# Performance work log

Hardware: AMD Instinct MI355X
Metric: run time of the kernel (lower is better)

The kernel has to match this reference:

```python
import jax, jax.numpy as jnp
import numpy as np

B, T, FDIM, H = 8, 2048, 512, 8
DK = FDIM // H
INF_VAL = 10000.0


def setup_inputs() -> dict:
    key = jax.random.key(0)
    ks = jax.random.split(key, 12)
    s = 1.0 / np.sqrt(FDIM)
    return {
        "query": jax.random.normal(ks[0], (B, T, FDIM), jnp.float32),
        "key": jax.random.normal(ks[1], (B, T, FDIM), jnp.float32),
        "value": jax.random.normal(ks[2], (B, T, FDIM), jnp.float32),
        "mask": jax.random.bernoulli(ks[3], 0.1, (B, T, T)),
        "Wq": jax.random.normal(ks[4], (FDIM, FDIM), jnp.float32) * s,
        "bq": jnp.zeros((FDIM,), jnp.float32),
        "Wk": jax.random.normal(ks[5], (FDIM, FDIM), jnp.float32) * s,
        "bk": jnp.zeros((FDIM,), jnp.float32),
        "Wv": jax.random.normal(ks[6], (FDIM, FDIM), jnp.float32) * s,
        "bv": jnp.zeros((FDIM,), jnp.float32),
        "Wo": jax.random.normal(ks[7], (FDIM, FDIM), jnp.float32) * s,
        "bo": jnp.zeros((FDIM,), jnp.float32),
    }


def reference(query, key, value, mask, Wq, bq, Wk, bk, Wv, bv, Wo, bo):
    # Linear projections (torch Linear: y = x W^T + b) then split heads.
    q = (query @ Wq.T + bq).reshape(B, T, H, DK).transpose(0, 2, 1, 3)  # (B,H,T1,DK)
    k = (key @ Wk.T + bk).reshape(B, T, H, DK).transpose(0, 2, 1, 3)    # (B,H,T2,DK)
    v = (value @ Wv.T + bv).reshape(B, T, H, DK).transpose(0, 2, 1, 3)  # (B,H,T2,DK)
    scores = jnp.einsum("bhqd,bhkd->bhqk", q, k) / jnp.sqrt(jnp.float32(DK))
    m = mask[:, None, :, :]  # (B,1,T1,T2)
    scores = jnp.where(m, -INF_VAL, scores)
    attn = jax.nn.softmax(scores, axis=-1)
    attn = jnp.where(m, 0.0, attn)
    # dropout_rate = 0.0 -> identity
    x = jnp.einsum("bhqk,bhkd->bhqd", attn, v)  # (B,H,T1,DK)
    x = x.transpose(0, 2, 1, 3).reshape(B, T, H * DK)
    return x @ Wo.T + bo
```

## Files before the change

kernel.cpp:

```cpp
#include <hip/hip_runtime.h>
#include <hip/hip_bf16.h>
#include <stdint.h>

#define B_N 8
#define T_N 2048
#define FDIM_N 512
#define H_N 8
#define DK_N 64

typedef float f32x4 __attribute__((ext_vector_type(4)));
typedef float float4v __attribute__((ext_vector_type(4)));
typedef __bf16 bf16x8 __attribute__((ext_vector_type(8)));
typedef unsigned short ushort8v __attribute__((ext_vector_type(8)));
typedef unsigned int uint2v __attribute__((ext_vector_type(2)));
typedef unsigned int uint4v __attribute__((ext_vector_type(4)));

#if __has_builtin(__builtin_amdgcn_exp2f)
#define EXP2F(x) __builtin_amdgcn_exp2f(x)
#else
#define EXP2F(x) exp2f(x)
#endif

static __device__ __forceinline__ unsigned short f2bf(float f) {
  unsigned int u = __builtin_bit_cast(unsigned int, f);
  u += 0x7fffu + ((u >> 16) & 1u);
  return (unsigned short)(u >> 16);
}

static __device__ __forceinline__ unsigned cvtpk(float lo, float hi) {
  unsigned r;
  asm("v_cvt_pk_bf16_f32 %0, %1, %2" : "=v"(r) : "v"(lo), "v"(hi));
  return r;
}

static __device__ __forceinline__ void gld_lds16(const void* g, void* l) {
  __builtin_amdgcn_global_load_lds(
      (const __attribute__((address_space(1))) unsigned int*)g,
      (__attribute__((address_space(3))) unsigned int*)l, 16, 0, 0);
}

static __device__ __forceinline__ bf16x8 ld_bf8(const unsigned short* p) {
  return *reinterpret_cast<const bf16x8*>(p);
}

#define SWZ8(row, colE) ((colE) ^ (((row) & 7) << 3))

#define QSCALE 0.1803368801111244f

__global__ __launch_bounds__(256) void prep_k(const int* __restrict__ m,
                                              const float* __restrict__ w0,
                                              const float* __restrict__ w1,
                                              const float* __restrict__ w2,
                                              const float* __restrict__ w3,
                                              unsigned short* __restrict__ wb,
                                              unsigned long long* __restrict__ mbits) {
  const int bid = blockIdx.x;
  if (bid < 2048) {
    const size_t n = (size_t)B_N * T_N * T_N;
    const size_t stride = (size_t)2048 * 256;
    for (size_t i = (size_t)bid * 256 + threadIdx.x; i < n; i += stride) {
      unsigned long long bl = __ballot(m[i] != 0);
      if ((threadIdx.x & 63) == 0) mbits[i >> 6] = bl;
    }
  } else {
    const int i = (bid - 2048) * 256 + threadIdx.x;
    const int ws = i >> 15, o = i & 32767;
    const float* w = (ws == 0) ? w0 : (ws == 1) ? w1 : (ws == 2) ? w2 : w3;
    const float4v a = *reinterpret_cast<const float4v*>(w + (size_t)o * 8);
    const float4v b = *reinterpret_cast<const float4v*>(w + (size_t)o * 8 + 4);
    const ushort8v out = {f2bf(a.x), f2bf(a.y), f2bf(a.z), f2bf(a.w),
                          f2bf(b.x), f2bf(b.y), f2bf(b.z), f2bf(b.w)};
    *reinterpret_cast<ushort8v*>(wb + (size_t)i * 8) = out;
  }
}

__global__ __launch_bounds__(256, 2) void proj_k(
    const float* __restrict__ qin, const float* __restrict__ kin, const float* __restrict__ vin,
    const unsigned short* __restrict__ wb, const float* __restrict__ bq,
    const float* __restrict__ bk, const float* __restrict__ bv,
    unsigned short* __restrict__ q_scr, unsigned short* __restrict__ k_scr,
    unsigned short* __restrict__ vT_scr) {
  __shared__ unsigned short As[128 * 64];
  __shared__ unsigned short Bs[128 * 64];
  const int tid = threadIdx.x;
  const int lane = tid & 63, w = tid >> 6;
  const int lr = lane & 15, lg = lane >> 4;
  const int swz_rd = (lr & 7) << 3;
  const int id = blockIdx.x;
  const int work = (id & 7) * 192 + (id >> 3);
  const int gb = work / 512;
  const int wk = work - gb * 512;
  const int m0 = (wk >> 2) * 128, n0 = (wk & 3) * 128;
  const int wm = (w & 1) * 64, wn = (w >> 1) * 64;

  const float* Ap = (gb == 0) ? qin : (gb == 1) ? kin : vin;
  const unsigned short* Wp = wb + (size_t)gb * 262144;
  const float* biasp = (gb == 0) ? bq : (gb == 1) ? bk : bv;

  f32x4 acc[4][4];
  const f32x4 z4 = {0.f, 0.f, 0.f, 0.f};
#pragma unroll
  for (int i = 0; i < 4; ++i)
#pragma unroll
    for (int j = 0; j < 4; ++j) acc[i][j] = z4;

  float4v areg[8];
#pragma unroll
  for (int j = 0; j < 8; ++j) {
    const int c = j * 256 + tid;
    areg[j] = *reinterpret_cast<const float4v*>(Ap + (size_t)(m0 + (c >> 4)) * 512 + (c & 15) * 4);
  }

  for (int k0 = 0; k0 < 512; k0 += 64) {
    __syncthreads();
#pragma unroll
    for (int j = 0; j < 8; ++j) {
      const int c = j * 256 + tid;
      const int row = c >> 4, g4 = c & 15;
      const uint2v pk = {cvtpk(areg[j].x, areg[j].y), cvtpk(areg[j].z, areg[j].w)};
      const int eo = row * 64 + (((g4 >> 1) * 8) ^ ((row & 7) << 3)) + (g4 & 1) * 4;
      *reinterpret_cast<uint2v*>(&As[eo]) = pk;
    }
#pragma unroll
    for (int i = 0; i < 4; ++i) {
      const int c = i * 256 + tid;
      const int row = c >> 3, ch = c & 7;
      gld_lds16(Wp + (size_t)(n0 + row) * 512 + k0 + SWZ8(row, ch * 8), &Bs[c * 8]);
    }
    if (k0 < 448) {
#pragma unroll
      for (int j = 0; j < 8; ++j) {
        const int c = j * 256 + tid;
        areg[j] = *reinterpret_cast<const float4v*>(Ap + (size_t)(m0 + (c >> 4)) * 512 + k0 + 64 +
                                                    (c & 15) * 4);
      }
    }
    __syncthreads();
    bf16x8 af[4][2], bw[4][2];
#pragma unroll
    for (int mt = 0; mt < 4; ++mt)
#pragma unroll
      for (int kk = 0; kk < 2; ++kk)
        af[mt][kk] = ld_bf8(&As[(wm + mt * 16 + lr) * 64 + ((kk * 32 + lg * 8) ^ swz_rd)]);
#pragma unroll
    for (int nt = 0; nt < 4; ++nt)
#pragma unroll
      for (int kk = 0; kk < 2; ++kk)
        bw[nt][kk] = ld_bf8(&Bs[(wn + nt * 16 + lr) * 64 + ((kk * 32 + lg * 8) ^ swz_rd)]);
#pragma unroll
    for (int kk = 0; kk < 2; ++kk)
#pragma unroll
      for (int mt = 0; mt < 4; ++mt)
#pragma unroll
        for (int nt = 0; nt < 4; ++nt)
          acc[mt][nt] =
              __builtin_amdgcn_mfma_f32_16x16x32_bf16(af[mt][kk], bw[nt][kk], acc[mt][nt], 0, 0, 0);
  }

#pragma unroll
  for (int nt = 0; nt < 4; ++nt) {
    const int n = n0 + wn + nt * 16 + lr;
    const float bias = biasp[n];
#pragma unroll
    for (int mt = 0; mt < 4; ++mt) {
#pragma unroll
      for (int j = 0; j < 4; ++j) {
        const int m = m0 + wm + mt * 16 + lg * 4 + j;
        float v = acc[mt][nt][j] + bias;
        const int bb = m >> 11, t = m & 2047;
        const int hh = n >> 6, d = n & 63;
        if (gb == 0) {
          v *= QSCALE;
          q_scr[(((size_t)(bb * 8 + hh) * 2048 + t) << 6) + d] = f2bf(v);
        } else if (gb == 1) {
          k_scr[(((size_t)(bb * 8 + hh) * 2048 + t) << 6) + d] = f2bf(v);
        } else {
          const int tp = (t & ~31) | (((t >> 2) & 3) << 3) | (((t >> 4) & 1) << 2) | (t & 3);
          vT_scr[(((size_t)(bb * 8 + hh) * 64 + d) << 11) + tp] = f2bf(v);
        }
      }
    }
  }
}

__global__ __launch_bounds__(256, 2) void attn_k(
    const unsigned short* __restrict__ qg, const unsigned short* __restrict__ kg,
    const unsigned short* __restrict__ vtg, const unsigned long long* __restrict__ mb,
    unsigned short* __restrict__ xg) {
  __shared__ unsigned short Ks[2][64 * 64];
  __shared__ unsigned short Vts[2][64 * 64];

  const int tid = threadIdx.x;
  const int lane = tid & 63, w = tid >> 6;
  const int lr = lane & 15, lg = lane >> 4;
  const int swz_rd = (lr & 7) << 3;
  const int id = blockIdx.x;
  const int work = (id & 7) * 128 + (id >> 3);
  const int bh = work >> 4, qt0 = work & 15;
  const int b = bh >> 3, h = bh & 7;
  const int q0 = qt0 * 128;

  bf16x8 aq[2][2];
#pragma unroll
  for (int qt = 0; qt < 2; ++qt)
#pragma unroll
    for (int kk = 0; kk < 2; ++kk)
      aq[qt][kk] =
          ld_bf8(qg + ((size_t)bh * T_N + q0 + w * 32 + qt * 16 + lr) * DK_N + kk * 32 + lg * 8);

  const int c0 = tid, c1 = 256 + tid;
  const int r0 = c0 >> 3, sw0 = SWZ8(r0, (c0 & 7) * 8);
  const int r1 = c1 >> 3, sw1 = SWZ8(r1, (c1 & 7) * 8);
  const unsigned short* kp0 = kg + (size_t)bh * (T_N * DK_N) + r0 * 64 + sw0;
  const unsigned short* kp1 = kg + (size_t)bh * (T_N * DK_N) + r1 * 64 + sw1;
  const unsigned short* vp0 = vtg + ((size_t)bh * DK_N + r0) * T_N + sw0;
  const unsigned short* vp1 = vtg + ((size_t)bh * DK_N + r1) * T_N + sw1;
  const unsigned long long* mp0 = mb + ((size_t)b * T_N + q0 + w * 32 + lr) * (T_N / 64);
  const unsigned long long* mp1 = mp0 + 16 * (T_N / 64);

  f32x4 OT[2][4];
  float l_run[2] = {0.f, 0.f};
  const f32x4 z4 = {0.f, 0.f, 0.f, 0.f};
#pragma unroll
  for (int qt = 0; qt < 2; ++qt)
#pragma unroll
    for (int dt = 0; dt < 4; ++dt) OT[qt][dt] = z4;

#define STAGE(PB)                       \
  {                                     \
    gld_lds16(kp0, &Ks[PB][c0 * 8]);    \
    gld_lds16(kp1, &Ks[PB][c1 * 8]);    \
    gld_lds16(vp0, &Vts[PB][c0 * 8]);   \
    gld_lds16(vp1, &Vts[PB][c1 * 8]);   \
    kp0 += 4096; kp1 += 4096; vp0 += 64; vp1 += 64; \
  }

  f32x4 ST[2][4];
  bf16x8 pfrag[2][2];
  unsigned long long mc0, mc1, mn0 = 0, mn1 = 0;

#define QKT_BLOCK(CUR)                                                                      \
  {                                                                                         \
    __builtin_amdgcn_s_setprio(1);                                                          \
    _Pragma("unroll") for (int st = 0; st < 4; ++st) {                                      \
      const bf16x8 kb0 = ld_bf8(&Ks[CUR][(st * 16 + lr) * 64 + ((lg * 8) ^ swz_rd)]);       \
      const bf16x8 kb1 = ld_bf8(&Ks[CUR][(st * 16 + lr) * 64 + ((32 + lg * 8) ^ swz_rd)]);  \
      _Pragma("unroll") for (int qt = 0; qt < 2; ++qt) {                                    \
        f32x4 a_ = __builtin_amdgcn_mfma_f32_16x16x32_bf16(kb0, aq[qt][0], z4, 0, 0, 0);    \
        ST[qt][st] = __builtin_amdgcn_mfma_f32_16x16x32_bf16(kb1, aq[qt][1], a_, 0, 0, 0);  \
      }                                                                                     \
    }                                                                                       \
    __builtin_amdgcn_s_setprio(0);                                                          \
  }

#define SOFTMAX_BLOCK()                                                                     \
  {                                                                                         \
    _Pragma("unroll") for (int qt = 0; qt < 2; ++qt) {                                      \
      const unsigned long long mrow = qt ? mc1 : mc0;                                       \
      float sv[4][4], rs4[4];                                                               \
      _Pragma("unroll") for (int st = 0; st < 4; ++st) {                                    \
        const unsigned nib = (unsigned)(mrow >> (st * 16 + lg * 4)) & 0xFu;                 \
        _Pragma("unroll") for (int j = 0; j < 4; ++j) {                                     \
          float e = EXP2F(ST[qt][st][j]);                                                   \
          e = ((nib >> j) & 1u) ? 0.f : e;                                                  \
          sv[st][j] = e;                                                                    \
        }                                                                                   \
        rs4[st] = (sv[st][0] + sv[st][1]) + (sv[st][2] + sv[st][3]);                        \
      }                                                                                     \
      float rs = (rs4[0] + rs4[1]) + (rs4[2] + rs4[3]);                                     \
      rs += __shfl_xor(rs, 16);                                                             \
      rs += __shfl_xor(rs, 32);                                                             \
      l_run[qt] += rs;                                                                      \
      uint4v pk0_, pk1_;                                                                    \
      pk0_.x = cvtpk(sv[0][0], sv[0][1]); pk0_.y = cvtpk(sv[0][2], sv[0][3]);               \
      pk0_.z = cvtpk(sv[1][0], sv[1][1]); pk0_.w = cvtpk(sv[1][2], sv[1][3]);               \
      pk1_.x = cvtpk(sv[2][0], sv[2][1]); pk1_.y = cvtpk(sv[2][2], sv[2][3]);               \
      pk1_.z = cvtpk(sv[3][0], sv[3][1]); pk1_.w = cvtpk(sv[3][2], sv[3][3]);               \
      pfrag[qt][0] = __builtin_bit_cast(bf16x8, pk0_);                                      \
      pfrag[qt][1] = __builtin_bit_cast(bf16x8, pk1_);                                      \
    }                                                                                       \
  }

#define PV_BLOCK(PRV)                                                                       \
  {                                                                                         \
    __builtin_amdgcn_s_setprio(1);                                                          \
    _Pragma("unroll") for (int dt = 0; dt < 4; ++dt) {                                      \
      const bf16x8 v0 = ld_bf8(&Vts[PRV][(dt * 16 + lr) * 64 + ((lg * 8) ^ swz_rd)]);       \
      const bf16x8 v1 = ld_bf8(&Vts[PRV][(dt * 16 + lr) * 64 + ((32 + lg * 8) ^ swz_rd)]);  \
      _Pragma("unroll") for (int qt = 0; qt < 2; ++qt) {                                    \
        f32x4 o_ = __builtin_amdgcn_mfma_f32_16x16x32_bf16(v0, pfrag[qt][0], OT[qt][dt], 0, 0, 0); \
        OT[qt][dt] = __builtin_amdgcn_mfma_f32_16x16x32_bf16(v1, pfrag[qt][1], o_, 0, 0, 0); \
      }                                                                                     \
    }                                                                                       \
    __builtin_amdgcn_s_setprio(0);                                                          \
  }

  STAGE(0);
  mc0 = mp0[0]; mc1 = mp1[0];
  __syncthreads();
  QKT_BLOCK(0);
  STAGE(1);
  mn0 = mp0[1]; mn1 = mp1[1];
  SOFTMAX_BLOCK();
  mc0 = mn0; mc1 = mn1;

#define ITER(KT, CUR, LAST)                     \
  {                                             \
    PV_BLOCK(CUR ^ 1);           \
    __syncthreads();                            \
    QKT_BLOCK(CUR);                \
    if (!(LAST)) {                              \
      STAGE(CUR ^ 1);            \
      mn0 = mp0[(KT) + 1]; mn1 = mp1[(KT) + 1]; \
    }                                           \
    SOFTMAX_BLOCK();             \
    mc0 = mn0; mc1 = mn1;                       \
  }

  ITER(1, 1, 0)
  for (int kt0 = 2; kt0 < 30; kt0 += 2) {
    ITER(kt0, 0, 0)
    ITER(kt0 + 1, 1, 0)
  }
  ITER(30, 0, 0)
  ITER(31, 1, 1)
  PV_BLOCK(1);
#undef ITER
#undef STAGE
#undef QKT_BLOCK
#undef SOFTMAX_BLOCK
#undef PV_BLOCK

#pragma unroll
  for (int qt = 0; qt < 2; ++qt) {
    const float l = l_run[qt];
    const float inv = (l > 0.f) ? 1.f / l : 0.f;
    const int q = q0 + w * 32 + qt * 16 + lr;
#pragma unroll
    for (int dt = 0; dt < 4; ++dt) {
      uint2v o;
      o.x = cvtpk(OT[qt][dt][0] * inv, OT[qt][dt][1] * inv);
      o.y = cvtpk(OT[qt][dt][2] * inv, OT[qt][dt][3] * inv);
      *reinterpret_cast<uint2v*>(xg + ((size_t)(b * T_N + q)) * FDIM_N + h * 64 + dt * 16 +
                                 lg * 4) = o;
    }
  }
}

__global__ __launch_bounds__(256, 3) void gemm_out_k(const unsigned short* __restrict__ Ap,
                                                     const unsigned short* __restrict__ Wp,
                                                     const float* __restrict__ biasp,
                                                     float* __restrict__ Cp) {
  __shared__ unsigned short As[128 * 64];
  __shared__ unsigned short Bs[128 * 64];
  const int tid = threadIdx.x;
  const int lane = tid & 63, w = tid >> 6;
  const int lr = lane & 15, lg = lane >> 4;
  const int id = blockIdx.x;
  const int work = (id & 7) * 64 + (id >> 3);
  const int m0 = (work >> 2) * 128, n0 = (work & 3) * 128;
  const int wm = (w & 1) * 64, wn = (w >> 1) * 64;
  const int swz_rd = (lr & 7) << 3;

  f32x4 acc[4][4];
  const f32x4 z4 = {0.f, 0.f, 0.f, 0.f};
#pragma unroll
  for (int i = 0; i < 4; ++i)
#pragma unroll
    for (int j = 0; j < 4; ++j) acc[i][j] = z4;

  for (int k0 = 0; k0 < 512; k0 += 64) {
    __syncthreads();
#pragma unroll
    for (int i = 0; i < 4; ++i) {
      const int c = i * 256 + tid;
      const int row = c >> 3, ch = c & 7;
      const int sw = SWZ8(row, ch * 8);
      gld_lds16(Ap + (size_t)(m0 + row) * 512 + k0 + sw, &As[c * 8]);
      gld_lds16(Wp + (size_t)(n0 + row) * 512 + k0 + sw, &Bs[c * 8]);
    }
    __syncthreads();
    bf16x8 af[4][2], bw[4][2];
#pragma unroll
    for (int mt = 0; mt < 4; ++mt)
#pragma unroll
      for (int kk = 0; kk < 2; ++kk)
        af[mt][kk] = ld_bf8(&As[(wm + mt * 16 + lr) * 64 + ((kk * 32 + lg * 8) ^ swz_rd)]);
#pragma unroll
    for (int nt = 0; nt < 4; ++nt)
#pragma unroll
      for (int kk = 0; kk < 2; ++kk)
        bw[nt][kk] = ld_bf8(&Bs[(wn + nt * 16 + lr) * 64 + ((kk * 32 + lg * 8) ^ swz_rd)]);
#pragma unroll
    for (int kk = 0; kk < 2; ++kk)
#pragma unroll
      for (int mt = 0; mt < 4; ++mt)
#pragma unroll
        for (int nt = 0; nt < 4; ++nt)
          acc[mt][nt] =
              __builtin_amdgcn_mfma_f32_16x16x32_bf16(af[mt][kk], bw[nt][kk], acc[mt][nt], 0, 0, 0);
  }

#pragma unroll
  for (int nt = 0; nt < 4; ++nt) {
    const int n = n0 + wn + nt * 16 + lr;
    const float bias = biasp[n];
#pragma unroll
    for (int mt = 0; mt < 4; ++mt) {
#pragma unroll
      for (int j = 0; j < 4; ++j) {
        const int m = m0 + wm + mt * 16 + lg * 4 + j;
        Cp[(size_t)m * 512 + n] = acc[mt][nt][j] + bias;
      }
    }
  }
}

extern "C" void kernel_launch(void* const* d_in, const int* in_sizes, int n_in,
                              void* d_out, int out_size, void* d_ws, size_t ws_size,
                              hipStream_t stream) {
  const float* query = (const float*)d_in[0];
  const float* key = (const float*)d_in[1];
  const float* value = (const float*)d_in[2];
  const int* mask = (const int*)d_in[3];
  const float* Wq = (const float*)d_in[4];
  const float* bq = (const float*)d_in[5];
  const float* Wk = (const float*)d_in[6];
  const float* bk = (const float*)d_in[7];
  const float* Wv = (const float*)d_in[8];
  const float* bv = (const float*)d_in[9];
  const float* Wo = (const float*)d_in[10];
  const float* bo = (const float*)d_in[11];

  const size_t NE = (size_t)16384 * 512;
  const size_t WE = (size_t)512 * 512;
  unsigned short* wqb = (unsigned short*)d_ws;
  unsigned short* q_scr = wqb + 4 * WE;
  unsigned short* k_scr = q_scr + NE;
  unsigned short* vT_scr = k_scr + NE;
  unsigned short* x_scr = vT_scr + NE;
  unsigned long long* mbits = (unsigned long long*)(x_scr + NE);

  prep_k<<<2560, 256, 0, stream>>>(mask, Wq, Wk, Wv, Wo, wqb, mbits);
  proj_k<<<1536, 256, 0, stream>>>(query, key, value, wqb, bq, bk, bv, q_scr, k_scr, vT_scr);
  attn_k<<<1024, 256, 0, stream>>>(q_scr, k_scr, vT_scr, mbits, x_scr);
  gemm_out_k<<<512, 256, 0, stream>>>(x_scr, wqb + 3 * WE, bo, (float*)d_out);
}
```

Before: 247.3 us.

## Double the attention KV tile to 128 keys and pre-permute mask bits

The attention kernel now stages 128 keys per iteration instead of 64, halving the number of barrier-separated pipeline steps. The PV product consumes two 64-key halves per stage. Mask bits are rearranged in the prep kernel so each lane reads a single 16-bit word of its own bits instead of extracting nibbles from a 64-bit row. Row-sum cross-lane shuffles are deferred to the epilogue. The cost is twice the LDS footprint (64KB total) and more live registers, which may lower occupancy.

```diff
diff --git a/kernel.cpp b/kernel.cpp
--- a/kernel.cpp
+++ b/kernel.cpp
@@ -60,7 +60,18 @@
     const size_t stride = (size_t)2048 * 256;
     for (size_t i = (size_t)bid * 256 + threadIdx.x; i < n; i += stride) {
       unsigned long long bl = __ballot(m[i] != 0);
-      if ((threadIdx.x & 63) == 0) mbits[i >> 6] = bl;
+      if ((threadIdx.x & 63) == 0) {
+        unsigned long long r = 0;
+#pragma unroll
+        for (int lg = 0; lg < 4; ++lg) {
+          unsigned v = 0;
+#pragma unroll
+          for (int st = 0; st < 4; ++st)
+            v |= (((unsigned)(bl >> (st * 16 + lg * 4)) & 0xFu) << (st * 4));
+          r |= (unsigned long long)v << (lg * 16);
+        }
+        mbits[i >> 6] = r;
+      }
     }
   } else {
     const int i = (bid - 2048) * 256 + threadIdx.x;
@@ -185,10 +196,10 @@
 
 __global__ __launch_bounds__(256, 2) void attn_k(
     const unsigned short* __restrict__ qg, const unsigned short* __restrict__ kg,
-    const unsigned short* __restrict__ vtg, const unsigned long long* __restrict__ mb,
+    const unsigned short* __restrict__ vtg, const unsigned short* __restrict__ mb16,
     unsigned short* __restrict__ xg) {
-  __shared__ unsigned short Ks[2][64 * 64];
-  __shared__ unsigned short Vts[2][64 * 64];
+  __shared__ unsigned short Ks[2][128 * 64];
+  __shared__ unsigned short Vts[2][64 * 128];
 
   const int tid = threadIdx.x;
   const int lane = tid & 63, w = tid >> 6;
@@ -208,132 +219,156 @@
       aq[qt][kk] =
           ld_bf8(qg + ((size_t)bh * T_N + q0 + w * 32 + qt * 16 + lr) * DK_N + kk * 32 + lg * 8);
 
-  const int c0 = tid, c1 = 256 + tid;
-  const int r0 = c0 >> 3, sw0 = SWZ8(r0, (c0 & 7) * 8);
-  const int r1 = c1 >> 3, sw1 = SWZ8(r1, (c1 & 7) * 8);
-  const unsigned short* kp0 = kg + (size_t)bh * (T_N * DK_N) + r0 * 64 + sw0;
-  const unsigned short* kp1 = kg + (size_t)bh * (T_N * DK_N) + r1 * 64 + sw1;
-  const unsigned short* vp0 = vtg + ((size_t)bh * DK_N + r0) * T_N + sw0;
-  const unsigned short* vp1 = vtg + ((size_t)bh * DK_N + r1) * T_N + sw1;
-  const unsigned long long* mp0 = mb + ((size_t)b * T_N + q0 + w * 32 + lr) * (T_N / 64);
-  const unsigned long long* mp1 = mp0 + 16 * (T_N / 64);
+  const unsigned short* kp[4];
+  const unsigned short* vp[4];
+#pragma unroll
+  for (int it = 0; it < 4; ++it) {
+    const int c = it * 256 + tid;
+    const int kr = c >> 3;
+    kp[it] = kg + (size_t)bh * (T_N * DK_N) + kr * 64 + SWZ8(kr, (c & 7) * 8);
+    const int vr = c >> 4;
+    vp[it] = vtg + ((size_t)bh * DK_N + vr) * T_N + SWZ8(vr, (c & 15) * 8);
+  }
+  const unsigned short* mq0 = mb16 + (size_t)(b * T_N + q0 + w * 32 + lr) * 128 + lg;
+  const unsigned short* mq1 = mq0 + (size_t)16 * 128;
 
   f32x4 OT[2][4];
-  float l_run[2] = {0.f, 0.f};
+  float rsacc[2] = {0.f, 0.f};
   const f32x4 z4 = {0.f, 0.f, 0.f, 0.f};
 #pragma unroll
   for (int qt = 0; qt < 2; ++qt)
 #pragma unroll
     for (int dt = 0; dt < 4; ++dt) OT[qt][dt] = z4;
 
-#define STAGE(PB)                       \
-  {                                     \
-    gld_lds16(kp0, &Ks[PB][c0 * 8]);    \
-    gld_lds16(kp1, &Ks[PB][c1 * 8]);    \
-    gld_lds16(vp0, &Vts[PB][c0 * 8]);   \
-    gld_lds16(vp1, &Vts[PB][c1 * 8]);   \
-    kp0 += 4096; kp1 += 4096; vp0 += 64; vp1 += 64; \
-  }
-
   f32x4 ST[2][4];
-  bf16x8 pfrag[2][2];
-  unsigned long long mc0, mc1, mn0 = 0, mn1 = 0;
-
-#define QKT_BLOCK(CUR)                                                                      \
-  {                                                                                         \
-    __builtin_amdgcn_s_setprio(1);                                                          \
-    _Pragma("unroll") for (int st = 0; st < 4; ++st) {                                      \
-      const bf16x8 kb0 = ld_bf8(&Ks[CUR][(st * 16 + lr) * 64 + ((lg * 8) ^ swz_rd)]);       \
-      const bf16x8 kb1 = ld_bf8(&Ks[CUR][(st * 16 + lr) * 64 + ((32 + lg * 8) ^ swz_rd)]);  \
-      _Pragma("unroll") for (int qt = 0; qt < 2; ++qt) {                                    \
-        f32x4 a_ = __builtin_amdgcn_mfma_f32_16x16x32_bf16(kb0, aq[qt][0], z4, 0, 0, 0);    \
-        ST[qt][st] = __builtin_amdgcn_mfma_f32_16x16x32_bf16(kb1, aq[qt][1], a_, 0, 0, 0);  \
-      }                                                                                     \
-    }                                                                                       \
-    __builtin_amdgcn_s_setprio(0);                                                          \
-  }
-
-#define SOFTMAX_BLOCK()                                                                     \
-  {                                                                                         \
-    _Pragma("unroll") for (int qt = 0; qt < 2; ++qt) {                                      \
-      const unsigned long long mrow = qt ? mc1 : mc0;                                       \
-      float sv[4][4], rs4[4];                                                               \
-      _Pragma("unroll") for (int st = 0; st < 4; ++st) {                                    \
-        const unsigned nib = (unsigned)(mrow >> (st * 16 + lg * 4)) & 0xFu;                 \
-        _Pragma("unroll") for (int j = 0; j < 4; ++j) {                                     \
-          float e = EXP2F(ST[qt][st][j]);                                                   \
-          e = ((nib >> j) & 1u) ? 0.f : e;                                                  \
-          sv[st][j] = e;                                                                    \
-        }                                                                                   \
-        rs4[st] = (sv[st][0] + sv[st][1]) + (sv[st][2] + sv[st][3]);                        \
-      }                                                                                     \
-      float rs = (rs4[0] + rs4[1]) + (rs4[2] + rs4[3]);                                     \
-      rs += __shfl_xor(rs, 16);                                                             \
-      rs += __shfl_xor(rs, 32);                                                             \
-      l_run[qt] += rs;                                                                      \
-      uint4v pk0_, pk1_;                                                                    \
-      pk0_.x = cvtpk(sv[0][0], sv[0][1]); pk0_.y = cvtpk(sv[0][2], sv[0][3]);               \
-      pk0_.z = cvtpk(sv[1][0], sv[1][1]); pk0_.w = cvtpk(sv[1][2], sv[1][3]);               \
-      pk1_.x = cvtpk(sv[2][0], sv[2][1]); pk1_.y = cvtpk(sv[2][2], sv[2][3]);               \
-      pk1_.z = cvtpk(sv[3][0], sv[3][1]); pk1_.w = cvtpk(sv[3][2], sv[3][3]);               \
-      pfrag[qt][0] = __builtin_bit_cast(bf16x8, pk0_);                                      \
-      pfrag[qt][1] = __builtin_bit_cast(bf16x8, pk1_);                                      \
-    }                                                                                       \
-  }
-
-#define PV_BLOCK(PRV)                                                                       \
-  {                                                                                         \
-    __builtin_amdgcn_s_setprio(1);                                                          \
-    _Pragma("unroll") for (int dt = 0; dt < 4; ++dt) {                                      \
-      const bf16x8 v0 = ld_bf8(&Vts[PRV][(dt * 16 + lr) * 64 + ((lg * 8) ^ swz_rd)]);       \
-      const bf16x8 v1 = ld_bf8(&Vts[PRV][(dt * 16 + lr) * 64 + ((32 + lg * 8) ^ swz_rd)]);  \
-      _Pragma("unroll") for (int qt = 0; qt < 2; ++qt) {                                    \
-        f32x4 o_ = __builtin_amdgcn_mfma_f32_16x16x32_bf16(v0, pfrag[qt][0], OT[qt][dt], 0, 0, 0); \
-        OT[qt][dt] = __builtin_amdgcn_mfma_f32_16x16x32_bf16(v1, pfrag[qt][1], o_, 0, 0, 0); \
-      }                                                                                     \
-    }                                                                                       \
-    __builtin_amdgcn_s_setprio(0);                                                          \
+  bf16x8 pfrag[2][2][2];
+  unsigned mc00, mc01, mc10, mc11, mn00 = 0, mn01 = 0, mn10 = 0, mn11 = 0;
+
+#define STAGE(PB)                                             \
+  {                                                           \
+    _Pragma("unroll") for (int it = 0; it < 4; ++it) {        \
+      gld_lds16(kp[it], &Ks[PB][(it * 256 + tid) * 8]);       \
+      kp[it] += 8192;                                         \
+    }                                                         \
+    _Pragma("unroll") for (int it = 0; it < 4; ++it) {        \
+      gld_lds16(vp[it], &Vts[PB][(it * 256 + tid) * 8]);      \
+      vp[it] += 128;                                          \
+    }                                                         \
+  }
+
+#define MLOAD_C(T) \
+  { mc00 = mq0[(T) * 8]; mc01 = mq0[(T) * 8 + 4]; mc10 = mq1[(T) * 8]; mc11 = mq1[(T) * 8 + 4]; }
+#define MLOAD_N(T) \
+  { mn00 = mq0[(T) * 8]; mn01 = mq0[(T) * 8 + 4]; mn10 = mq1[(T) * 8]; mn11 = mq1[(T) * 8 + 4]; }
+
+#define QKT_H(CUR, HH)                                                                       \
+  {                                                                                          \
+    __builtin_amdgcn_s_setprio(1);                                                           \
+    _Pragma("unroll") for (int st = 0; st < 4; ++st) {                                       \
+      const int krow = (HH) * 64 + st * 16 + lr;                                             \
+      const bf16x8 kb0 = ld_bf8(&Ks[CUR][krow * 64 + ((lg * 8) ^ swz_rd)]);                  \
+      const bf16x8 kb1 = ld_bf8(&Ks[CUR][krow * 64 + ((32 + lg * 8) ^ swz_rd)]);             \
+      _Pragma("unroll") for (int qt = 0; qt < 2; ++qt) {                                     \
+        f32x4 a_ = __builtin_amdgcn_mfma_f32_16x16x32_bf16(kb0, aq[qt][0], z4, 0, 0, 0);     \
+        ST[qt][st] = __builtin_amdgcn_mfma_f32_16x16x32_bf16(kb1, aq[qt][1], a_, 0, 0, 0);   \
+      }                                                                                      \
+    }                                                                                        \
+    __builtin_amdgcn_s_setprio(0);                                                           \
+  }
+
+#define SOFTMAX_H(HH, MS0, MS1)                                                              \
+  {                                                                                          \
+    _Pragma("unroll") for (int qt = 0; qt < 2; ++qt) {                                       \
+      const unsigned ms = qt ? (MS1) : (MS0);                                                \
+      float sv[4][4];                                                                        \
+      _Pragma("unroll") for (int st = 0; st < 4; ++st) {                                     \
+        const unsigned nib = (ms >> (st * 4)) & 0xFu;                                        \
+        _Pragma("unroll") for (int j = 0; j < 4; ++j) {                                      \
+          float e = EXP2F(ST[qt][st][j]);                                                    \
+          e = ((nib >> j) & 1u) ? 0.f : e;                                                   \
+          sv[st][j] = e;                                                                     \
+        }                                                                                    \
+      }                                                                                      \
+      rsacc[qt] += ((sv[0][0] + sv[0][1]) + (sv[0][2] + sv[0][3])) +                         \
+                   ((sv[1][0] + sv[1][1]) + (sv[1][2] + sv[1][3])) +                         \
+                   ((sv[2][0] + sv[2][1]) + (sv[2][2] + sv[2][3])) +                         \
+                   ((sv[3][0] + sv[3][1]) + (sv[3][2] + sv[3][3]));                          \
+      uint4v pk0_, pk1_;                                                                     \
+      pk0_.x = cvtpk(sv[0][0], sv[0][1]); pk0_.y = cvtpk(sv[0][2], sv[0][3]);                \
+      pk0_.z = cvtpk(sv[1][0], sv[1][1]); pk0_.w = cvtpk(sv[1][2], sv[1][3]);                \
+      pk1_.x = cvtpk(sv[2][0], sv[2][1]); pk1_.y = cvtpk(sv[2][2], sv[2][3]);                \
+      pk1_.z = cvtpk(sv[3][0], sv[3][1]); pk1_.w = cvtpk(sv[3][2], sv[3][3]);                \
+      pfrag[qt][HH][0] = __builtin_bit_cast(bf16x8, pk0_);                                   \
+      pfrag[qt][HH][1] = __builtin_bit_cast(bf16x8, pk1_);                                   \
+    }                                                                                        \
+  }
+
+#define PV_BLOCK(PRV)                                                                        \
+  {                                                                                          \
+    __builtin_amdgcn_s_setprio(1);                                                           \
+    _Pragma("unroll") for (int dt = 0; dt < 4; ++dt) {                                       \
+      const int vrow = (dt * 16 + lr) * 128;                                                 \
+      _Pragma("unroll") for (int hh = 0; hh < 2; ++hh) {                                     \
+        const bf16x8 v0 = ld_bf8(&Vts[PRV][vrow + ((hh * 64 + lg * 8) ^ swz_rd)]);           \
+        const bf16x8 v1 = ld_bf8(&Vts[PRV][vrow + ((hh * 64 + 32 + lg * 8) ^ swz_rd)]);      \
+        _Pragma("unroll") for (int qt = 0; qt < 2; ++qt) {                                   \
+          f32x4 o_ =                                                                         \
+              __builtin_amdgcn_mfma_f32_16x16x32_bf16(v0, pfrag[qt][hh][0], OT[qt][dt], 0, 0, 0); \
+          OT[qt][dt] =                                                                       \
+              __builtin_amdgcn_mfma_f32_16x16x32_bf16(v1, pfrag[qt][hh][1], o_, 0, 0, 0);    \
+        }                                                                                    \
+      }                                                                                      \
+    }                                                                                        \
+    __builtin_amdgcn_s_setprio(0);                                                           \
   }
 
   STAGE(0);
-  mc0 = mp0[0]; mc1 = mp1[0];
+  MLOAD_C(0);
   __syncthreads();
-  QKT_BLOCK(0);
+  QKT_H(0, 0);
   STAGE(1);
-  mn0 = mp0[1]; mn1 = mp1[1];
-  SOFTMAX_BLOCK();
-  mc0 = mn0; mc1 = mn1;
-
-#define ITER(KT, CUR, LAST)                     \
+  MLOAD_N(1);
+  SOFTMAX_H(0, mc00, mc10);
+  QKT_H(0, 1);
+  SOFTMAX_H(1, mc01, mc11);
+  mc00 = mn00; mc01 = mn01; mc10 = mn10; mc11 = mn11;
+
+#define ITER(T, CUR, LAST)                      \
   {                                             \
-    PV_BLOCK(CUR ^ 1);           \
+    PV_BLOCK(CUR ^ 1);            \
     __syncthreads();                            \
-    QKT_BLOCK(CUR);                \
+    QKT_H(CUR, 0);          \
     if (!(LAST)) {                              \
-      STAGE(CUR ^ 1);            \
-      mn0 = mp0[(KT) + 1]; mn1 = mp1[(KT) + 1]; \
+      STAGE(CUR ^ 1);             \
+      MLOAD_N((T) + 1);                         \
     }                                           \
-    SOFTMAX_BLOCK();             \
-    mc0 = mn0; mc1 = mn1;                       \
+    SOFTMAX_H(0, mc00, mc10);                   \
+    QKT_H(CUR, 1);          \
+    SOFTMAX_H(1, mc01, mc11);                   \
+    mc00 = mn00; mc01 = mn01; mc10 = mn10; mc11 = mn11; \
   }
 
   ITER(1, 1, 0)
-  for (int kt0 = 2; kt0 < 30; kt0 += 2) {
-    ITER(kt0, 0, 0)
-    ITER(kt0 + 1, 1, 0)
-  }
-  ITER(30, 0, 0)
-  ITER(31, 1, 1)
+  for (int T = 2; T < 14; T += 2) {
+    ITER(T, 0, 0)
+    ITER(T + 1, 1, 0)
+  }
+  ITER(14, 0, 0)
+  ITER(15, 1, 1)
   PV_BLOCK(1);
 #undef ITER
 #undef STAGE
-#undef QKT_BLOCK
-#undef SOFTMAX_BLOCK
+#undef MLOAD_C
+#undef MLOAD_N
+#undef QKT_H
+#undef SOFTMAX_H
 #undef PV_BLOCK
 
 #pragma unroll
   for (int qt = 0; qt < 2; ++qt) {
-    const float l = l_run[qt];
+    float l = rsacc[qt];
+    l += __shfl_xor(l, 16);
+    l += __shfl_xor(l, 32);
     const float inv = (l > 0.f) ? 1.f / l : 0.f;
     const int q = q0 + w * 32 + qt * 16 + lr;
 #pragma unroll
@@ -443,6 +478,6 @@
 
   prep_k<<<2560, 256, 0, stream>>>(mask, Wq, Wk, Wv, Wo, wqb, mbits);
   proj_k<<<1536, 256, 0, stream>>>(query, key, value, wqb, bq, bk, bv, q_scr, k_scr, vT_scr);
-  attn_k<<<1024, 256, 0, stream>>>(q_scr, k_scr, vT_scr, mbits, x_scr);
+  attn_k<<<1024, 256, 0, stream>>>(q_scr, k_scr, vT_scr, (const unsigned short*)mbits, x_scr);
   gemm_out_k<<<512, 256, 0, stream>>>(x_scr, wqb + 3 * WE, bo, (float*)d_out);
 }
```

After: 260.6 us. 5.4% more time.

## Split attention work across eight waves with one query tile each

Applied to the files above, without the earlier changes.

The attention kernel now runs 512 threads per block, and each of the eight waves handles 16 query rows instead of 32. Each thread stages one K and one V chunk per tile instead of two. The row sum is now accumulated per lane and reduced across lanes only once at the end, rather than shuffled every tile. This is meant to raise wave-level parallelism and cut per-thread registers and cross-lane shuffles, at the cost of halving MFMA work per LDS fragment load and syncing more waves at each barrier.

```diff
diff --git a/kernel.cpp b/kernel.cpp
--- a/kernel.cpp
+++ b/kernel.cpp
@@ -183,7 +183,7 @@
   }
 }
 
-__global__ __launch_bounds__(256, 2) void attn_k(
+__global__ __launch_bounds__(512, 4) void attn_k(
     const unsigned short* __restrict__ qg, const unsigned short* __restrict__ kg,
     const unsigned short* __restrict__ vtg, const unsigned long long* __restrict__ mb,
     unsigned short* __restrict__ xg) {
@@ -200,44 +200,34 @@
   const int b = bh >> 3, h = bh & 7;
   const int q0 = qt0 * 128;
 
-  bf16x8 aq[2][2];
-#pragma unroll
-  for (int qt = 0; qt < 2; ++qt)
-#pragma unroll
-    for (int kk = 0; kk < 2; ++kk)
-      aq[qt][kk] =
-          ld_bf8(qg + ((size_t)bh * T_N + q0 + w * 32 + qt * 16 + lr) * DK_N + kk * 32 + lg * 8);
-
-  const int c0 = tid, c1 = 256 + tid;
-  const int r0 = c0 >> 3, sw0 = SWZ8(r0, (c0 & 7) * 8);
-  const int r1 = c1 >> 3, sw1 = SWZ8(r1, (c1 & 7) * 8);
-  const unsigned short* kp0 = kg + (size_t)bh * (T_N * DK_N) + r0 * 64 + sw0;
-  const unsigned short* kp1 = kg + (size_t)bh * (T_N * DK_N) + r1 * 64 + sw1;
-  const unsigned short* vp0 = vtg + ((size_t)bh * DK_N + r0) * T_N + sw0;
-  const unsigned short* vp1 = vtg + ((size_t)bh * DK_N + r1) * T_N + sw1;
-  const unsigned long long* mp0 = mb + ((size_t)b * T_N + q0 + w * 32 + lr) * (T_N / 64);
-  const unsigned long long* mp1 = mp0 + 16 * (T_N / 64);
-
-  f32x4 OT[2][4];
-  float l_run[2] = {0.f, 0.f};
+  bf16x8 aq[2];
+#pragma unroll
+  for (int kk = 0; kk < 2; ++kk)
+    aq[kk] = ld_bf8(qg + ((size_t)bh * T_N + q0 + w * 16 + lr) * DK_N + kk * 32 + lg * 8);
+
+  const int krow = tid >> 3, kch = tid & 7;
+  const unsigned short* kp =
+      kg + (size_t)bh * (T_N * DK_N) + krow * 64 + SWZ8(krow, kch * 8);
+  const unsigned short* vp =
+      vtg + ((size_t)bh * DK_N + krow) * T_N + SWZ8(krow, kch * 8);
+  const unsigned long long* mp = mb + ((size_t)b * T_N + q0 + w * 16 + lr) * (T_N / 64);
+
+  f32x4 OT[4];
+  float rsacc = 0.f;
   const f32x4 z4 = {0.f, 0.f, 0.f, 0.f};
 #pragma unroll
-  for (int qt = 0; qt < 2; ++qt)
-#pragma unroll
-    for (int dt = 0; dt < 4; ++dt) OT[qt][dt] = z4;
-
-#define STAGE(PB)                       \
-  {                                     \
-    gld_lds16(kp0, &Ks[PB][c0 * 8]);    \
-    gld_lds16(kp1, &Ks[PB][c1 * 8]);    \
-    gld_lds16(vp0, &Vts[PB][c0 * 8]);   \
-    gld_lds16(vp1, &Vts[PB][c1 * 8]);   \
-    kp0 += 4096; kp1 += 4096; vp0 += 64; vp1 += 64; \
-  }
-
-  f32x4 ST[2][4];
-  bf16x8 pfrag[2][2];
-  unsigned long long mc0, mc1, mn0 = 0, mn1 = 0;
+  for (int dt = 0; dt < 4; ++dt) OT[dt] = z4;
+
+  f32x4 ST[4];
+  bf16x8 pfrag[2];
+  unsigned long long mc, mn = 0;
+
+#define STAGE(PB)                        \
+  {                                      \
+    gld_lds16(kp, &Ks[PB][tid * 8]);     \
+    gld_lds16(vp, &Vts[PB][tid * 8]);    \
+    kp += 4096; vp += 64;                \
+  }
 
 #define QKT_BLOCK(CUR)                                                                      \
   {                                                                                         \
@@ -245,40 +235,34 @@
     _Pragma("unroll") for (int st = 0; st < 4; ++st) {                                      \
       const bf16x8 kb0 = ld_bf8(&Ks[CUR][(st * 16 + lr) * 64 + ((lg * 8) ^ swz_rd)]);       \
       const bf16x8 kb1 = ld_bf8(&Ks[CUR][(st * 16 + lr) * 64 + ((32 + lg * 8) ^ swz_rd)]);  \
-      _Pragma("unroll") for (int qt = 0; qt < 2; ++qt) {                                    \
-        f32x4 a_ = __builtin_amdgcn_mfma_f32_16x16x32_bf16(kb0, aq[qt][0], z4, 0, 0, 0);    \
-        ST[qt][st] = __builtin_amdgcn_mfma_f32_16x16x32_bf16(kb1, aq[qt][1], a_, 0, 0, 0);  \
+      f32x4 a_ = __builtin_amdgcn_mfma_f32_16x16x32_bf16(kb0, aq[0], z4, 0, 0, 0);          \
+      ST[st] = __builtin_amdgcn_mfma_f32_16x16x32_bf16(kb1, aq[1], a_, 0, 0, 0);            \
+    }                                                                                       \
+    __builtin_amdgcn_s_setprio(0);                                                          \
+  }
+
+#define SOFTMAX_BLOCK()                                                                     \
+  {                                                                                         \
+    float sv[4][4];                                                                         \
+    _Pragma("unroll") for (int st = 0; st < 4; ++st) {                                      \
+      const unsigned nib = (unsigned)(mc >> (st * 16 + lg * 4)) & 0xFu;                     \
+      _Pragma("unroll") for (int j = 0; j < 4; ++j) {                                       \
+        float e = EXP2F(ST[st][j]);                                                         \
+        e = ((nib >> j) & 1u) ? 0.f : e;                                                    \
+        sv[st][j] = e;                                                                      \
       }                                                                                     \
     }                                                                                       \
-    __builtin_amdgcn_s_setprio(0);                                                          \
-  }
-
-#define SOFTMAX_BLOCK()                                                                     \
-  {                                                                                         \
-    _Pragma("unroll") for (int qt = 0; qt < 2; ++qt) {                                      \
-      const unsigned long long mrow = qt ? mc1 : mc0;                                       \
-      float sv[4][4], rs4[4];                                                               \
-      _Pragma("unroll") for (int st = 0; st < 4; ++st) {                                    \
-        const unsigned nib = (unsigned)(mrow >> (st * 16 + lg * 4)) & 0xFu;                 \
-        _Pragma("unroll") for (int j = 0; j < 4; ++j) {                                     \
-          float e = EXP2F(ST[qt][st][j]);                                                   \
-          e = ((nib >> j) & 1u) ? 0.f : e;                                                  \
-          sv[st][j] = e;                                                                    \
-        }                                                                                   \
-        rs4[st] = (sv[st][0] + sv[st][1]) + (sv[st][2] + sv[st][3]);                        \
-      }                                                                                     \
-      float rs = (rs4[0] + rs4[1]) + (rs4[2] + rs4[3]);                                     \
-      rs += __shfl_xor(rs, 16);                                                             \
-      rs += __shfl_xor(rs, 32);                                                             \
-      l_run[qt] += rs;                                                                      \
-      uint4v pk0_, pk1_;                                                                    \
-      pk0_.x = cvtpk(sv[0][0], sv[0][1]); pk0_.y = cvtpk(sv[0][2], sv[0][3]);               \
-      pk0_.z = cvtpk(sv[1][0], sv[1][1]); pk0_.w = cvtpk(sv[1][2], sv[1][3]);               \
-      pk1_.x = cvtpk(sv[2][0], sv[2][1]); pk1_.y = cvtpk(sv[2][2], sv[2][3]);               \
-      pk1_.z = cvtpk(sv[3][0], sv[3][1]); pk1_.w = cvtpk(sv[3][2], sv[3][3]);               \
-      pfrag[qt][0] = __builtin_bit_cast(bf16x8, pk0_);                                      \
-      pfrag[qt][1] = __builtin_bit_cast(bf16x8, pk1_);                                      \
-    }                                                                                       \
+    rsacc += (((sv[0][0] + sv[0][1]) + (sv[0][2] + sv[0][3])) +                             \
+              ((sv[1][0] + sv[1][1]) + (sv[1][2] + sv[1][3]))) +                            \
+             (((sv[2][0] + sv[2][1]) + (sv[2][2] + sv[2][3])) +                             \
+              ((sv[3][0] + sv[3][1]) + (sv[3][2] + sv[3][3])));                             \
+    uint4v pk0_, pk1_;                                                                      \
+    pk0_.x = cvtpk(sv[0][0], sv[0][1]); pk0_.y = cvtpk(sv[0][2], sv[0][3]);                 \
+    pk0_.z = cvtpk(sv[1][0], sv[1][1]); pk0_.w = cvtpk(sv[1][2], sv[1][3]);                 \
+    pk1_.x = cvtpk(sv[2][0], sv[2][1]); pk1_.y = cvtpk(sv[2][2], sv[2][3]);                 \
+    pk1_.z = cvtpk(sv[3][0], sv[3][1]); pk1_.w = cvtpk(sv[3][2], sv[3][3]);                 \
+    pfrag[0] = __builtin_bit_cast(bf16x8, pk0_);                                            \
+    pfrag[1] = __builtin_bit_cast(bf16x8, pk1_);                                            \
   }
 
 #define PV_BLOCK(PRV)                                                                       \
@@ -287,34 +271,32 @@
     _Pragma("unroll") for (int dt = 0; dt < 4; ++dt) {                                      \
       const bf16x8 v0 = ld_bf8(&Vts[PRV][(dt * 16 + lr) * 64 + ((lg * 8) ^ swz_rd)]);       \
       const bf16x8 v1 = ld_bf8(&Vts[PRV][(dt * 16 + lr) * 64 + ((32 + lg * 8) ^ swz_rd)]);  \
-      _Pragma("unroll") for (int qt = 0; qt < 2; ++qt) {                                    \
-        f32x4 o_ = __builtin_amdgcn_mfma_f32_16x16x32_bf16(v0, pfrag[qt][0], OT[qt][dt], 0, 0, 0); \
-        OT[qt][dt] = __builtin_amdgcn_mfma_f32_16x16x32_bf16(v1, pfrag[qt][1], o_, 0, 0, 0); \
-      }                                                                                     \
+      f32x4 o_ = __builtin_amdgcn_mfma_f32_16x16x32_bf16(v0, pfrag[0], OT[dt], 0, 0, 0);    \
+      OT[dt] = __builtin_amdgcn_mfma_f32_16x16x32_bf16(v1, pfrag[1], o_, 0, 0, 0);          \
     }                                                                                       \
     __builtin_amdgcn_s_setprio(0);                                                          \
   }
 
   STAGE(0);
-  mc0 = mp0[0]; mc1 = mp1[0];
+  mc = mp[0];
   __syncthreads();
   QKT_BLOCK(0);
   STAGE(1);
-  mn0 = mp0[1]; mn1 = mp1[1];
+  mn = mp[1];
   SOFTMAX_BLOCK();
-  mc0 = mn0; mc1 = mn1;
-
-#define ITER(KT, CUR, LAST)                     \
-  {                                             \
-    PV_BLOCK(CUR ^ 1);           \
-    __syncthreads();                            \
-    QKT_BLOCK(CUR);                \
-    if (!(LAST)) {                              \
-      STAGE(CUR ^ 1);            \
-      mn0 = mp0[(KT) + 1]; mn1 = mp1[(KT) + 1]; \
-    }                                           \
-    SOFTMAX_BLOCK();             \
-    mc0 = mn0; mc1 = mn1;                       \
+  mc = mn;
+
+#define ITER(KT, CUR, LAST)            \
+  {                                    \
+    PV_BLOCK(CUR ^ 1);  \
+    __syncthreads();                   \
+    QKT_BLOCK(CUR);       \
+    if (!(LAST)) {                     \
+      STAGE(CUR ^ 1);   \
+      mn = mp[(KT) + 1];               \
+    }                                  \
+    SOFTMAX_BLOCK();    \
+    mc = mn;                           \
   }
 
   ITER(1, 1, 0)
@@ -331,16 +313,17 @@
 #undef SOFTMAX_BLOCK
 #undef PV_BLOCK
 
-#pragma unroll
-  for (int qt = 0; qt < 2; ++qt) {
-    const float l = l_run[qt];
+  {
+    float l = rsacc;
+    l += __shfl_xor(l, 16);
+    l += __shfl_xor(l, 32);
     const float inv = (l > 0.f) ? 1.f / l : 0.f;
-    const int q = q0 + w * 32 + qt * 16 + lr;
+    const int q = q0 + w * 16 + lr;
 #pragma unroll
     for (int dt = 0; dt < 4; ++dt) {
       uint2v o;
-      o.x = cvtpk(OT[qt][dt][0] * inv, OT[qt][dt][1] * inv);
-      o.y = cvtpk(OT[qt][dt][2] * inv, OT[qt][dt][3] * inv);
+      o.x = cvtpk(OT[dt][0] * inv, OT[dt][1] * inv);
+      o.y = cvtpk(OT[dt][2] * inv, OT[dt][3] * inv);
       *reinterpret_cast<uint2v*>(xg + ((size_t)(b * T_N + q)) * FDIM_N + h * 64 + dt * 16 +
                                  lg * 4) = o;
     }
@@ -443,6 +426,6 @@
 
   prep_k<<<2560, 256, 0, stream>>>(mask, Wq, Wk, Wv, Wo, wqb, mbits);
   proj_k<<<1536, 256, 0, stream>>>(query, key, value, wqb, bq, bk, bv, q_scr, k_scr, vT_scr);
-  attn_k<<<1024, 256, 0, stream>>>(q_scr, k_scr, vT_scr, mbits, x_scr);
+  attn_k<<<1024, 512, 0, stream>>>(q_scr, k_scr, vT_scr, mbits, x_scr);
   gemm_out_k<<<512, 256, 0, stream>>>(x_scr, wqb + 3 * WE, bo, (float*)d_out);
 }
```

New measurement: 235.7 us. 4.7% less time.
